# Kernel optimization log

Hardware: AMD Instinct MI355X
Metric: run time of the kernel (lower is better)

## Reference

```python
import jax, jax.numpy as jnp
import numpy as np

B, LC, LQ, D = 64, 512, 64, 256

def setup_inputs() -> dict:
    key = jax.random.key(0)
    k1, k2, k3, k4 = jax.random.split(key, 4)
    contex = jax.random.normal(k1, (B, LC, D), dtype=jnp.float32)
    question = jax.random.normal(k2, (B, LQ, D), dtype=jnp.float32)
    W_weight = jax.random.normal(k3, (1, 3 * D), dtype=jnp.float32) * (1.0 / np.sqrt(3 * D))
    W_bias = jax.random.normal(k4, (1,), dtype=jnp.float32) * 0.01
    return {"contex": contex, "question": question, "W_weight": W_weight, "W_bias": W_bias}

def reference(contex, question, W_weight, W_bias):
    d = contex.shape[-1]
    w = W_weight[0]  # [3D]; cat order in original is [q, c, q*c]
    wq, wc, wi = w[:d], w[d:2 * d], w[2 * d:]
    # S[b,i,j] = c_i.wc + q_j.wq + (c_i*q_j).wi + bias  (trilinear decomposition)
    s_c = contex @ wc                                   # [B, Lc]
    s_q = question @ wq                                 # [B, Lq]
    s_i = jnp.einsum('bid,bjd->bij', contex * wi, question)  # [B, Lc, Lq]
    S = s_i + s_c[:, :, None] + s_q[:, None, :] + W_bias[0]
    S1 = jax.nn.softmax(S, axis=2)                      # over question
    S2 = jax.nn.softmax(S, axis=1)                      # over context
    A = jnp.einsum('bij,bjd->bid', S1, question)        # [B, Lc, D]
    S3 = jnp.einsum('bij,bkj->bik', S1, S2)             # [B, Lc, Lc]
    Bm = jnp.einsum('bik,bkd->bid', S3, contex)         # [B, Lc, D]
    out = jnp.concatenate([contex, A, contex * A, contex * Bm], axis=2)  # [B, Lc, 4D]
    return out  # dropout is identity at inference
```

## Files before the change

kernel.cpp:

```cpp
#include <hip/hip_runtime.h>

#define BB 64
#define LCC 512
#define LQQ 64
#define DDD 256

typedef short bf16x8 __attribute__((ext_vector_type(8)));
typedef float f32x4 __attribute__((ext_vector_type(4)));

__device__ __forceinline__ unsigned short f2bf(float f) {
  union { float f; unsigned u; } v; v.f = f;
  unsigned u = v.u;
  return (unsigned short)((u + 0x7fffu + ((u >> 16) & 1u)) >> 16);
}
__device__ __forceinline__ float bf2f(unsigned u16) {
  union { unsigned u; float f; } v; v.u = u16 << 16;
  return v.f;
}

__global__ __launch_bounds__(256) void k1_scores(
    const float* __restrict__ cx, const float* __restrict__ qu,
    const float* __restrict__ W, const float* __restrict__ Wb,
    unsigned short* __restrict__ E, unsigned short* __restrict__ Et,
    float* __restrict__ rinv)
{
  __shared__ float w_lds[768];
  __shared__ unsigned short As[128 * 72];
  __shared__ unsigned short Bs[64 * 72];
  __shared__ float E_lds[128 * 65];
  __shared__ float sc_lds[128];
  __shared__ float sq_lds[64];

  const int tid = threadIdx.x;
  const int b  = blockIdx.x >> 2;
  const int i0 = (blockIdx.x & 3) * 128;
  const int w = tid >> 6, lane = tid & 63, quad = lane >> 4, ln = lane & 15;

  for (int idx = tid; idx < 768; idx += 256) w_lds[idx] = W[idx];

  f32x4 acc[2][4];
#pragma unroll
  for (int a = 0; a < 2; ++a)
#pragma unroll
    for (int c = 0; c < 4; ++c) acc[a][c] = (f32x4){0.f, 0.f, 0.f, 0.f};

  float scp = 0.f;
  float sqp = 0.f;
  const int ai = tid >> 1, ah = tid & 1;
  const int bj = tid >> 2, bc = tid & 3;

  for (int kk = 0; kk < 4; ++kk) {
    __syncthreads();
    {
      const float4* src = (const float4*)(cx + ((size_t)(b * LCC + i0 + ai)) * DDD + kk * 64 + ah * 32);
      const float* wi = w_lds + 512 + kk * 64 + ah * 32;
      const float* wc = w_lds + 256 + kk * 64 + ah * 32;
      unsigned short* dst = As + ai * 72 + ah * 32;
#pragma unroll
      for (int u = 0; u < 8; ++u) {
        float4 v = src[u];
        scp += v.x * wc[u*4+0] + v.y * wc[u*4+1] + v.z * wc[u*4+2] + v.w * wc[u*4+3];
        ushort4 o;
        o.x = f2bf(v.x * wi[u*4+0]);
        o.y = f2bf(v.y * wi[u*4+1]);
        o.z = f2bf(v.z * wi[u*4+2]);
        o.w = f2bf(v.w * wi[u*4+3]);
        *(ushort4*)(dst + u * 4) = o;
      }
    }
    {
      const float4* src = (const float4*)(qu + ((size_t)(b * LQQ + bj)) * DDD + kk * 64 + bc * 16);
      const float* wq = w_lds + kk * 64 + bc * 16;
      unsigned short* dst = Bs + bj * 72 + bc * 16;
#pragma unroll
      for (int u = 0; u < 4; ++u) {
        float4 v = src[u];
        sqp += v.x * wq[u*4+0] + v.y * wq[u*4+1] + v.z * wq[u*4+2] + v.w * wq[u*4+3];
        ushort4 o = { f2bf(v.x), f2bf(v.y), f2bf(v.z), f2bf(v.w) };
        *(ushort4*)(dst + u * 4) = o;
      }
    }
    __syncthreads();
#pragma unroll
    for (int ks = 0; ks < 2; ++ks) {
      bf16x8 af[2];
#pragma unroll
      for (int tm = 0; tm < 2; ++tm)
        af[tm] = *(const bf16x8*)(As + (w * 32 + tm * 16 + ln) * 72 + ks * 32 + quad * 8);
#pragma unroll
      for (int tn = 0; tn < 4; ++tn) {
        bf16x8 bf = *(const bf16x8*)(Bs + (tn * 16 + ln) * 72 + ks * 32 + quad * 8);
#pragma unroll
        for (int tm = 0; tm < 2; ++tm)
          acc[tm][tn] = __builtin_amdgcn_mfma_f32_16x16x32_bf16(af[tm], bf, acc[tm][tn], 0, 0, 0);
      }
    }
  }

  __syncthreads();
  w_lds[tid] = scp;
  w_lds[256 + tid] = sqp;
  __syncthreads();
  if (tid < 128) sc_lds[tid] = w_lds[2*tid] + w_lds[2*tid+1];
  if (tid < 64)
    sq_lds[tid] = w_lds[256 + 4*tid] + w_lds[256 + 4*tid+1]
                + w_lds[256 + 4*tid+2] + w_lds[256 + 4*tid+3];
  const float bias = Wb[0];
  __syncthreads();

#pragma unroll
  for (int tm = 0; tm < 2; ++tm)
#pragma unroll
    for (int tn = 0; tn < 4; ++tn)
#pragma unroll
      for (int r = 0; r < 4; ++r) {
        int il = w * 32 + tm * 16 + quad * 4 + r;
        int j  = tn * 16 + ln;
        float e = __expf(acc[tm][tn][r] + sc_lds[il] + sq_lds[j] + bias);
        E_lds[il * 65 + j] = e;
      }
  __syncthreads();
  {
    float s = 0.f;
#pragma unroll
    for (int j = 0; j < 32; ++j) s += E_lds[ai * 65 + ah * 32 + j];
    w_lds[tid] = s;
  }
  __syncthreads();
  if (tid < 128) rinv[b * LCC + i0 + tid] = 1.0f / (w_lds[2*tid] + w_lds[2*tid+1]);

  {
    unsigned short* dst = E + ((size_t)(b * LCC + i0 + ai)) * 64 + ah * 32;
    const float* srcr = E_lds + ai * 65 + ah * 32;
#pragma unroll
    for (int u = 0; u < 8; ++u) {
      ushort4 o = { f2bf(srcr[u*4+0]), f2bf(srcr[u*4+1]), f2bf(srcr[u*4+2]), f2bf(srcr[u*4+3]) };
      *(ushort4*)(dst + u * 4) = o;
    }
  }
  {
    unsigned short* dst = Et + ((size_t)(b * LQQ + bj)) * LCC + i0 + bc * 32;
#pragma unroll
    for (int u = 0; u < 8; ++u) {
      ushort4 o;
      o.x = f2bf(E_lds[(bc*32 + u*4 + 0) * 65 + bj]);
      o.y = f2bf(E_lds[(bc*32 + u*4 + 1) * 65 + bj]);
      o.z = f2bf(E_lds[(bc*32 + u*4 + 2) * 65 + bj]);
      o.w = f2bf(E_lds[(bc*32 + u*4 + 3) * 65 + bj]);
      *(ushort4*)(dst + u * 4) = o;
    }
  }
}

__global__ __launch_bounds__(256) void k2_tmat(
    const float* __restrict__ cx, const float* __restrict__ qu,
    const unsigned short* __restrict__ Et,
    unsigned short* __restrict__ Qt, unsigned short* __restrict__ Tt)
{
  __shared__ unsigned short As2[64 * 72];
  __shared__ unsigned short Bs2[64 * 72];
  __shared__ float Tl[64 * 65];
  __shared__ float cs_lds[64];

  const int tid = threadIdx.x;
  const int b  = blockIdx.x >> 2;
  const int d0 = (blockIdx.x & 3) * 64;
  const int w = tid >> 6, lane = tid & 63, quad = lane >> 4, ln = lane & 15;

  {
    const int j = tid >> 2, c = tid & 3;
    const float4* src = (const float4*)(qu + ((size_t)(b * LQQ + j)) * DDD + d0 + c * 16);
#pragma unroll
    for (int u = 0; u < 4; ++u) {
      float4 v = src[u];
      Tl[j * 65 + c*16 + u*4 + 0] = v.x;
      Tl[j * 65 + c*16 + u*4 + 1] = v.y;
      Tl[j * 65 + c*16 + u*4 + 2] = v.z;
      Tl[j * 65 + c*16 + u*4 + 3] = v.w;
    }
  }
  __syncthreads();
  {
    const int d = tid & 63, cj = tid >> 6;
    unsigned short* dst = Qt + ((size_t)(b * DDD + d0 + d)) * 64 + cj * 16;
#pragma unroll
    for (int u = 0; u < 4; ++u) {
      ushort4 o;
      o.x = f2bf(Tl[(cj*16 + u*4 + 0) * 65 + d]);
      o.y = f2bf(Tl[(cj*16 + u*4 + 1) * 65 + d]);
      o.z = f2bf(Tl[(cj*16 + u*4 + 2) * 65 + d]);
      o.w = f2bf(Tl[(cj*16 + u*4 + 3) * 65 + d]);
      *(ushort4*)(dst + u * 4) = o;
    }
  }

  f32x4 acc[4];
#pragma unroll
  for (int c = 0; c < 4; ++c) acc[c] = (f32x4){0.f, 0.f, 0.f, 0.f};
  float csp = 0.f;

  const int sj = tid >> 2, sc = tid & 3;
  const int si = tid & 63, sc2 = tid >> 6;

  for (int kk = 0; kk < 8; ++kk) {
    __syncthreads();
    {
      const uint4* src = (const uint4*)(Et + ((size_t)(b * LQQ + sj)) * LCC + kk * 64 + sc * 16);
#pragma unroll
      for (int u = 0; u < 2; ++u) {
        uint4 raw = src[u];
        *(uint4*)(As2 + sj * 72 + sc * 16 + u * 8) = raw;
        csp += bf2f(raw.x & 0xffffu) + bf2f(raw.x >> 16)
             + bf2f(raw.y & 0xffffu) + bf2f(raw.y >> 16)
             + bf2f(raw.z & 0xffffu) + bf2f(raw.z >> 16)
             + bf2f(raw.w & 0xffffu) + bf2f(raw.w >> 16);
      }
    }
    {
      const float4* src = (const float4*)(cx + ((size_t)(b * LCC + kk * 64 + si)) * DDD + d0 + sc2 * 16);
#pragma unroll
      for (int u = 0; u < 4; ++u) {
        float4 v = src[u];
        Bs2[(sc2*16 + u*4 + 0) * 72 + si] = f2bf(v.x);
        Bs2[(sc2*16 + u*4 + 1) * 72 + si] = f2bf(v.y);
        Bs2[(sc2*16 + u*4 + 2) * 72 + si] = f2bf(v.z);
        Bs2[(sc2*16 + u*4 + 3) * 72 + si] = f2bf(v.w);
      }
    }
    __syncthreads();
#pragma unroll
    for (int ks = 0; ks < 2; ++ks) {
      bf16x8 af = *(const bf16x8*)(As2 + (w * 16 + ln) * 72 + ks * 32 + quad * 8);
#pragma unroll
      for (int tn = 0; tn < 4; ++tn) {
        bf16x8 bf = *(const bf16x8*)(Bs2 + (tn * 16 + ln) * 72 + ks * 32 + quad * 8);
        acc[tn] = __builtin_amdgcn_mfma_f32_16x16x32_bf16(af, bf, acc[tn], 0, 0, 0);
      }
    }
  }

  __syncthreads();
  Tl[tid] = csp;
  __syncthreads();
  if (tid < 64) {
    float s = Tl[4*tid] + Tl[4*tid+1] + Tl[4*tid+2] + Tl[4*tid+3];
    cs_lds[tid] = 1.0f / s;
  }
  __syncthreads();
#pragma unroll
  for (int tn = 0; tn < 4; ++tn)
#pragma unroll
    for (int r = 0; r < 4; ++r) {
      int jl = w * 16 + quad * 4 + r;
      Tl[jl * 65 + tn * 16 + ln] = acc[tn][r] * cs_lds[jl];
    }
  __syncthreads();
  {
    const int d = tid & 63, cj = tid >> 6;
    unsigned short* dst = Tt + ((size_t)(b * DDD + d0 + d)) * 64 + cj * 16;
#pragma unroll
    for (int u = 0; u < 4; ++u) {
      ushort4 o;
      o.x = f2bf(Tl[(cj*16 + u*4 + 0) * 65 + d]);
      o.y = f2bf(Tl[(cj*16 + u*4 + 1) * 65 + d]);
      o.z = f2bf(Tl[(cj*16 + u*4 + 2) * 65 + d]);
      o.w = f2bf(Tl[(cj*16 + u*4 + 3) * 65 + d]);
      *(ushort4*)(dst + u * 4) = o;
    }
  }
}

__global__ __launch_bounds__(256) void k3_out(
    const float* __restrict__ cx,
    const unsigned short* __restrict__ E,
    const unsigned short* __restrict__ Qt,
    const unsigned short* __restrict__ Tt,
    const float* __restrict__ rinv,
    float* __restrict__ out)
{
  __shared__ unsigned short As3[64 * 72];
  __shared__ char BsTr[256 * 72 * 2];
  __shared__ float ri_lds[64];
  unsigned short* Bs3 = (unsigned short*)BsTr;
  float* Tr = (float*)BsTr;

  const int tid = threadIdx.x;
  const int bid = blockIdx.x;
  const int b    = bid >> 4;
  const int it   = (bid >> 1) & 7;
  const int half = bid & 1;
  const int i0 = it * 64;
  const int w = tid >> 6, lane = tid & 63, quad = lane >> 4, ln = lane & 15;

  {
    const int i = tid >> 2, c = tid & 3;
    const uint4* src = (const uint4*)(E + ((size_t)(b * LCC + i0 + i)) * 64 + c * 16);
#pragma unroll
    for (int u = 0; u < 2; ++u)
      *(uint4*)(As3 + i * 72 + c * 16 + u * 8) = src[u];
  }
  {
    const unsigned short* Bsrc = half ? Tt : Qt;
    const int nb = tid & 63, c2 = tid >> 6;
#pragma unroll
    for (int rr = 0; rr < 4; ++rr) {
      int n = rr * 64 + nb;
      const uint4* src = (const uint4*)(Bsrc + ((size_t)(b * DDD + n)) * 64 + c2 * 16);
#pragma unroll
      for (int u = 0; u < 2; ++u)
        *(uint4*)(Bs3 + n * 72 + c2 * 16 + u * 8) = src[u];
    }
  }
  if (tid < 64) ri_lds[tid] = rinv[b * LCC + i0 + tid];
  __syncthreads();

  f32x4 acc[4][4];
#pragma unroll
  for (int a = 0; a < 4; ++a)
#pragma unroll
    for (int c = 0; c < 4; ++c) acc[a][c] = (f32x4){0.f, 0.f, 0.f, 0.f};

#pragma unroll
  for (int ks = 0; ks < 2; ++ks) {
    bf16x8 af[4], bf[4];
#pragma unroll
    for (int tm = 0; tm < 4; ++tm)
      af[tm] = *(const bf16x8*)(As3 + (tm * 16 + ln) * 72 + ks * 32 + quad * 8);
#pragma unroll
    for (int tn = 0; tn < 4; ++tn)
      bf[tn] = *(const bf16x8*)(Bs3 + (w * 64 + tn * 16 + ln) * 72 + ks * 32 + quad * 8);
#pragma unroll
    for (int tm = 0; tm < 4; ++tm)
#pragma unroll
      for (int tn = 0; tn < 4; ++tn)
        acc[tm][tn] = __builtin_amdgcn_mfma_f32_16x16x32_bf16(af[tm], bf[tn], acc[tm][tn], 0, 0, 0);
  }

  const float* cxb = cx + (size_t)b * LCC * DDD;
  float* ob = out + (size_t)b * LCC * 1024;
  const int row = tid >> 4;
  const int fq  = tid & 15;

#pragma unroll
  for (int tm = 0; tm < 4; ++tm) {
    __syncthreads();
#pragma unroll
    for (int tn = 0; tn < 4; ++tn)
#pragma unroll
      for (int r = 0; r < 4; ++r) {
        int rloc = quad * 4 + r;
        Tr[rloc * 260 + w * 64 + tn * 16 + ln] = acc[tm][tn][r] * ri_lds[tm * 16 + rloc];
      }
    __syncthreads();
    const int i = i0 + tm * 16 + row;
#pragma unroll
    for (int u = 0; u < 4; ++u) {
      int c0 = (fq + u * 16) * 4;
      float4 v = *(const float4*)(Tr + row * 260 + c0);
      float4 c = *(const float4*)(cxb + (size_t)i * DDD + c0);
      float4 cv = { c.x * v.x, c.y * v.y, c.z * v.z, c.w * v.w };
      if (half == 0) {
        *(float4*)(ob + (size_t)i * 1024 + 256 + c0) = v;
        *(float4*)(ob + (size_t)i * 1024 + 512 + c0) = cv;
      } else {
        *(float4*)(ob + (size_t)i * 1024 + c0)       = c;
        *(float4*)(ob + (size_t)i * 1024 + 768 + c0) = cv;
      }
    }
  }
}

extern "C" void kernel_launch(void* const* d_in, const int* in_sizes, int n_in,
                              void* d_out, int out_size, void* d_ws, size_t ws_size,
                              hipStream_t stream) {
  const float* cx = (const float*)d_in[0];
  const float* qu = (const float*)d_in[1];
  const float* W  = (const float*)d_in[2];
  const float* Wb = (const float*)d_in[3];
  float* out = (float*)d_out;

  char* wsb = (char*)d_ws;
  unsigned short* E   = (unsigned short*)(wsb);
  unsigned short* Et  = (unsigned short*)(wsb + (4ull << 20));
  unsigned short* Qt  = (unsigned short*)(wsb + (8ull << 20));
  unsigned short* Tt  = (unsigned short*)(wsb + (10ull << 20));
  float*          ri  = (float*)(wsb + (12ull << 20));

  k1_scores<<<dim3(256), dim3(256), 0, stream>>>(cx, qu, W, Wb, E, Et, ri);
  k2_tmat  <<<dim3(256), dim3(256), 0, stream>>>(cx, qu, Et, Qt, Tt);
  k3_out   <<<dim3(1024), dim3(256), 0, stream>>>(cx, E, Qt, Tt, ri, out);
}
```

Baseline: 199.6 us.

## Double grid sizes of score and T kernels and load MFMA fragments directly from global

The score and T-matrix kernels now use 512 blocks with half-size tiles: 64 context rows per block in k1 and 32 feature columns per block in k2. k1 stages all of the question tile in LDS once, then each lane loads its context A fragment straight from global memory and converts it to bf16 in registers, so the per-k LDS staging loop and its barriers are gone. k2 and k3 also read their E/Et/Qt/Tt MFMA fragments directly from global instead of staging them in LDS. The intent is more parallelism and fewer barriers and LDS round trips. The cost is less coalesced, strided global fragment loads and some repeated loads across blocks.

Result: no change. 198.9 us (-0.4%).

```diff
diff --git a/kernel.cpp b/kernel.cpp
--- a/kernel.cpp
+++ b/kernel.cpp
@@ -8,13 +8,13 @@
 typedef short bf16x8 __attribute__((ext_vector_type(8)));
 typedef float f32x4 __attribute__((ext_vector_type(4)));
 
-__device__ __forceinline__ unsigned short f2bf(float f) {
+static __device__ __forceinline__ unsigned short f2bf(float f) {
   union { float f; unsigned u; } v; v.f = f;
   unsigned u = v.u;
   return (unsigned short)((u + 0x7fffu + ((u >> 16) & 1u)) >> 16);
 }
-__device__ __forceinline__ float bf2f(unsigned u16) {
-  union { unsigned u; float f; } v; v.u = u16 << 16;
+static __device__ __forceinline__ float bf2f(unsigned u16) {
+  union { unsigned u; float f; } v; v.u = (u16 & 0xffffu) << 16;
   return v.f;
 }
 
@@ -25,128 +25,118 @@
     float* __restrict__ rinv)
 {
   __shared__ float w_lds[768];
-  __shared__ unsigned short As[128 * 72];
-  __shared__ unsigned short Bs[64 * 72];
-  __shared__ float E_lds[128 * 65];
-  __shared__ float sc_lds[128];
+  __shared__ unsigned short Bs[64 * 264];
+  __shared__ float E_lds[64 * 65];
+  __shared__ float red[256];
+  __shared__ float sc_lds[64];
   __shared__ float sq_lds[64];
 
   const int tid = threadIdx.x;
-  const int b  = blockIdx.x >> 2;
-  const int i0 = (blockIdx.x & 3) * 128;
+  const int b  = blockIdx.x >> 3;
+  const int i0 = (blockIdx.x & 7) * 64;
   const int w = tid >> 6, lane = tid & 63, quad = lane >> 4, ln = lane & 15;
 
   for (int idx = tid; idx < 768; idx += 256) w_lds[idx] = W[idx];
-
-  f32x4 acc[2][4];
-#pragma unroll
-  for (int a = 0; a < 2; ++a)
-#pragma unroll
-    for (int c = 0; c < 4; ++c) acc[a][c] = (f32x4){0.f, 0.f, 0.f, 0.f};
+  __syncthreads();
+
+  {
+    const int bj = tid >> 2, bc = tid & 3;
+    const float4* src = (const float4*)(qu + ((size_t)(b * LQQ + bj)) * DDD + bc * 64);
+    const float* wq = w_lds + bc * 64;
+    unsigned short* dst = Bs + bj * 264 + bc * 64;
+    float sqp = 0.f;
+#pragma unroll
+    for (int u = 0; u < 16; ++u) {
+      float4 v = src[u];
+      sqp += v.x * wq[u*4+0] + v.y * wq[u*4+1] + v.z * wq[u*4+2] + v.w * wq[u*4+3];
+      ushort4 o = { f2bf(v.x), f2bf(v.y), f2bf(v.z), f2bf(v.w) };
+      *(ushort4*)(dst + u * 4) = o;
+    }
+    red[tid] = sqp;
+  }
+  __syncthreads();
+  if (tid < 64) sq_lds[tid] = red[4*tid] + red[4*tid+1] + red[4*tid+2] + red[4*tid+3];
+
+  f32x4 acc[4];
+#pragma unroll
+  for (int c = 0; c < 4; ++c) acc[c] = (f32x4){0.f, 0.f, 0.f, 0.f};
 
   float scp = 0.f;
-  float sqp = 0.f;
-  const int ai = tid >> 1, ah = tid & 1;
-  const int bj = tid >> 2, bc = tid & 3;
-
-  for (int kk = 0; kk < 4; ++kk) {
-    __syncthreads();
-    {
-      const float4* src = (const float4*)(cx + ((size_t)(b * LCC + i0 + ai)) * DDD + kk * 64 + ah * 32);
-      const float* wi = w_lds + 512 + kk * 64 + ah * 32;
-      const float* wc = w_lds + 256 + kk * 64 + ah * 32;
-      unsigned short* dst = As + ai * 72 + ah * 32;
-#pragma unroll
-      for (int u = 0; u < 8; ++u) {
-        float4 v = src[u];
-        scp += v.x * wc[u*4+0] + v.y * wc[u*4+1] + v.z * wc[u*4+2] + v.w * wc[u*4+3];
-        ushort4 o;
-        o.x = f2bf(v.x * wi[u*4+0]);
-        o.y = f2bf(v.y * wi[u*4+1]);
-        o.z = f2bf(v.z * wi[u*4+2]);
-        o.w = f2bf(v.w * wi[u*4+3]);
-        *(ushort4*)(dst + u * 4) = o;
+  const float* cxrow = cx + ((size_t)(b * LCC + i0 + w * 16 + ln)) * DDD;
+#pragma unroll
+  for (int kk = 0; kk < 4; ++kk)
+#pragma unroll
+    for (int ks = 0; ks < 2; ++ks) {
+      const int k0 = kk * 64 + ks * 32 + quad * 8;
+      float4 c0 = *(const float4*)(cxrow + k0);
+      float4 c1 = *(const float4*)(cxrow + k0 + 4);
+      const float* wcp = w_lds + 256 + k0;
+      const float* wip = w_lds + 512 + k0;
+      scp += c0.x*wcp[0] + c0.y*wcp[1] + c0.z*wcp[2] + c0.w*wcp[3]
+           + c1.x*wcp[4] + c1.y*wcp[5] + c1.z*wcp[6] + c1.w*wcp[7];
+      bf16x8 af;
+      af[0] = (short)f2bf(c0.x * wip[0]);
+      af[1] = (short)f2bf(c0.y * wip[1]);
+      af[2] = (short)f2bf(c0.z * wip[2]);
+      af[3] = (short)f2bf(c0.w * wip[3]);
+      af[4] = (short)f2bf(c1.x * wip[4]);
+      af[5] = (short)f2bf(c1.y * wip[5]);
+      af[6] = (short)f2bf(c1.z * wip[6]);
+      af[7] = (short)f2bf(c1.w * wip[7]);
+#pragma unroll
+      for (int tn = 0; tn < 4; ++tn) {
+        bf16x8 bf = *(const bf16x8*)(Bs + (tn * 16 + ln) * 264 + k0);
+        acc[tn] = __builtin_amdgcn_mfma_f32_16x16x32_bf16(af, bf, acc[tn], 0, 0, 0);
       }
     }
-    {
-      const float4* src = (const float4*)(qu + ((size_t)(b * LQQ + bj)) * DDD + kk * 64 + bc * 16);
-      const float* wq = w_lds + kk * 64 + bc * 16;
-      unsigned short* dst = Bs + bj * 72 + bc * 16;
-#pragma unroll
-      for (int u = 0; u < 4; ++u) {
-        float4 v = src[u];
-        sqp += v.x * wq[u*4+0] + v.y * wq[u*4+1] + v.z * wq[u*4+2] + v.w * wq[u*4+3];
-        ushort4 o = { f2bf(v.x), f2bf(v.y), f2bf(v.z), f2bf(v.w) };
-        *(ushort4*)(dst + u * 4) = o;
-      }
-    }
-    __syncthreads();
-#pragma unroll
-    for (int ks = 0; ks < 2; ++ks) {
-      bf16x8 af[2];
-#pragma unroll
-      for (int tm = 0; tm < 2; ++tm)
-        af[tm] = *(const bf16x8*)(As + (w * 32 + tm * 16 + ln) * 72 + ks * 32 + quad * 8);
-#pragma unroll
-      for (int tn = 0; tn < 4; ++tn) {
-        bf16x8 bf = *(const bf16x8*)(Bs + (tn * 16 + ln) * 72 + ks * 32 + quad * 8);
-#pragma unroll
-        for (int tm = 0; tm < 2; ++tm)
-          acc[tm][tn] = __builtin_amdgcn_mfma_f32_16x16x32_bf16(af[tm], bf, acc[tm][tn], 0, 0, 0);
-      }
-    }
-  }
-
-  __syncthreads();
-  w_lds[tid] = scp;
-  w_lds[256 + tid] = sqp;
-  __syncthreads();
-  if (tid < 128) sc_lds[tid] = w_lds[2*tid] + w_lds[2*tid+1];
+
+  __syncthreads();
+  red[(w * 16 + ln) * 4 + quad] = scp;
+  __syncthreads();
   if (tid < 64)
-    sq_lds[tid] = w_lds[256 + 4*tid] + w_lds[256 + 4*tid+1]
-                + w_lds[256 + 4*tid+2] + w_lds[256 + 4*tid+3];
-  const float bias = Wb[0];
-  __syncthreads();
-
-#pragma unroll
-  for (int tm = 0; tm < 2; ++tm)
-#pragma unroll
-    for (int tn = 0; tn < 4; ++tn)
-#pragma unroll
-      for (int r = 0; r < 4; ++r) {
-        int il = w * 32 + tm * 16 + quad * 4 + r;
-        int j  = tn * 16 + ln;
-        float e = __expf(acc[tm][tn][r] + sc_lds[il] + sq_lds[j] + bias);
-        E_lds[il * 65 + j] = e;
-      }
-  __syncthreads();
-  {
+    sc_lds[tid] = red[4*tid] + red[4*tid+1] + red[4*tid+2] + red[4*tid+3] + Wb[0];
+  __syncthreads();
+
+#pragma unroll
+  for (int tn = 0; tn < 4; ++tn)
+#pragma unroll
+    for (int r = 0; r < 4; ++r) {
+      int il = w * 16 + quad * 4 + r;
+      int j  = tn * 16 + ln;
+      E_lds[il * 65 + j] = __expf(acc[tn][r] + sc_lds[il] + sq_lds[j]);
+    }
+  __syncthreads();
+  {
+    const int i = tid >> 2, c = tid & 3;
     float s = 0.f;
 #pragma unroll
-    for (int j = 0; j < 32; ++j) s += E_lds[ai * 65 + ah * 32 + j];
-    w_lds[tid] = s;
-  }
-  __syncthreads();
-  if (tid < 128) rinv[b * LCC + i0 + tid] = 1.0f / (w_lds[2*tid] + w_lds[2*tid+1]);
-
-  {
-    unsigned short* dst = E + ((size_t)(b * LCC + i0 + ai)) * 64 + ah * 32;
-    const float* srcr = E_lds + ai * 65 + ah * 32;
-#pragma unroll
-    for (int u = 0; u < 8; ++u) {
+    for (int j = 0; j < 16; ++j) s += E_lds[i * 65 + c * 16 + j];
+    red[tid] = s;
+  }
+  __syncthreads();
+  if (tid < 64)
+    rinv[b * LCC + i0 + tid] = 1.0f / (red[4*tid] + red[4*tid+1] + red[4*tid+2] + red[4*tid+3]);
+
+  {
+    const int i = tid >> 2, c = tid & 3;
+    unsigned short* dst = E + ((size_t)(b * LCC + i0 + i)) * 64 + c * 16;
+    const float* srcr = E_lds + i * 65 + c * 16;
+#pragma unroll
+    for (int u = 0; u < 4; ++u) {
       ushort4 o = { f2bf(srcr[u*4+0]), f2bf(srcr[u*4+1]), f2bf(srcr[u*4+2]), f2bf(srcr[u*4+3]) };
       *(ushort4*)(dst + u * 4) = o;
     }
   }
   {
-    unsigned short* dst = Et + ((size_t)(b * LQQ + bj)) * LCC + i0 + bc * 32;
-#pragma unroll
-    for (int u = 0; u < 8; ++u) {
+    const int j = tid >> 2, c = tid & 3;
+    unsigned short* dst = Et + ((size_t)(b * LQQ + j)) * LCC + i0 + c * 16;
+#pragma unroll
+    for (int u = 0; u < 4; ++u) {
       ushort4 o;
-      o.x = f2bf(E_lds[(bc*32 + u*4 + 0) * 65 + bj]);
-      o.y = f2bf(E_lds[(bc*32 + u*4 + 1) * 65 + bj]);
-      o.z = f2bf(E_lds[(bc*32 + u*4 + 2) * 65 + bj]);
-      o.w = f2bf(E_lds[(bc*32 + u*4 + 3) * 65 + bj]);
+      o.x = f2bf(E_lds[(c*16 + u*4 + 0) * 65 + j]);
+      o.y = f2bf(E_lds[(c*16 + u*4 + 1) * 65 + j]);
+      o.z = f2bf(E_lds[(c*16 + u*4 + 2) * 65 + j]);
+      o.w = f2bf(E_lds[(c*16 + u*4 + 3) * 65 + j]);
       *(ushort4*)(dst + u * 4) = o;
     }
   }
@@ -157,116 +147,97 @@
     const unsigned short* __restrict__ Et,
     unsigned short* __restrict__ Qt, unsigned short* __restrict__ Tt)
 {
-  __shared__ unsigned short As2[64 * 72];
-  __shared__ unsigned short Bs2[64 * 72];
-  __shared__ float Tl[64 * 65];
-  __shared__ float cs_lds[64];
+  __shared__ unsigned short Bs2[32 * 72];
+  __shared__ float Tl[64 * 37];
+  __shared__ float red2[256];
+  __shared__ float csinv[64];
 
   const int tid = threadIdx.x;
-  const int b  = blockIdx.x >> 2;
-  const int d0 = (blockIdx.x & 3) * 64;
+  const int b  = blockIdx.x >> 3;
+  const int d0 = (blockIdx.x & 7) * 32;
   const int w = tid >> 6, lane = tid & 63, quad = lane >> 4, ln = lane & 15;
 
   {
     const int j = tid >> 2, c = tid & 3;
-    const float4* src = (const float4*)(qu + ((size_t)(b * LQQ + j)) * DDD + d0 + c * 16);
-#pragma unroll
-    for (int u = 0; u < 4; ++u) {
-      float4 v = src[u];
-      Tl[j * 65 + c*16 + u*4 + 0] = v.x;
-      Tl[j * 65 + c*16 + u*4 + 1] = v.y;
-      Tl[j * 65 + c*16 + u*4 + 2] = v.z;
-      Tl[j * 65 + c*16 + u*4 + 3] = v.w;
-    }
-  }
-  __syncthreads();
-  {
-    const int d = tid & 63, cj = tid >> 6;
-    unsigned short* dst = Qt + ((size_t)(b * DDD + d0 + d)) * 64 + cj * 16;
-#pragma unroll
-    for (int u = 0; u < 4; ++u) {
-      ushort4 o;
-      o.x = f2bf(Tl[(cj*16 + u*4 + 0) * 65 + d]);
-      o.y = f2bf(Tl[(cj*16 + u*4 + 1) * 65 + d]);
-      o.z = f2bf(Tl[(cj*16 + u*4 + 2) * 65 + d]);
-      o.w = f2bf(Tl[(cj*16 + u*4 + 3) * 65 + d]);
-      *(ushort4*)(dst + u * 4) = o;
-    }
-  }
-
-  f32x4 acc[4];
-#pragma unroll
-  for (int c = 0; c < 4; ++c) acc[c] = (f32x4){0.f, 0.f, 0.f, 0.f};
+    const float* srow = qu + ((size_t)(b * LQQ + j)) * DDD + d0 + c * 8;
+    float4 v0 = *(const float4*)srow;
+    float4 v1 = *(const float4*)(srow + 4);
+    float* t = Tl + j * 37 + c * 8;
+    t[0]=v0.x; t[1]=v0.y; t[2]=v0.z; t[3]=v0.w;
+    t[4]=v1.x; t[5]=v1.y; t[6]=v1.z; t[7]=v1.w;
+  }
+  __syncthreads();
+  {
+    const int d = tid >> 3, cj = tid & 7;
+    unsigned short* dst = Qt + ((size_t)(b * DDD + d0 + d)) * 64 + cj * 8;
+    ushort4 o0 = { f2bf(Tl[(cj*8+0)*37+d]), f2bf(Tl[(cj*8+1)*37+d]),
+                   f2bf(Tl[(cj*8+2)*37+d]), f2bf(Tl[(cj*8+3)*37+d]) };
+    ushort4 o1 = { f2bf(Tl[(cj*8+4)*37+d]), f2bf(Tl[(cj*8+5)*37+d]),
+                   f2bf(Tl[(cj*8+6)*37+d]), f2bf(Tl[(cj*8+7)*37+d]) };
+    *(ushort4*)dst = o0;
+    *(ushort4*)(dst + 4) = o1;
+  }
+
+  f32x4 acc[2];
+  acc[0] = (f32x4){0.f, 0.f, 0.f, 0.f};
+  acc[1] = (f32x4){0.f, 0.f, 0.f, 0.f};
   float csp = 0.f;
-
-  const int sj = tid >> 2, sc = tid & 3;
+  const unsigned short* etrow = Et + ((size_t)(b * LQQ + w * 16 + ln)) * LCC;
   const int si = tid & 63, sc2 = tid >> 6;
 
   for (int kk = 0; kk < 8; ++kk) {
     __syncthreads();
     {
-      const uint4* src = (const uint4*)(Et + ((size_t)(b * LQQ + sj)) * LCC + kk * 64 + sc * 16);
-#pragma unroll
-      for (int u = 0; u < 2; ++u) {
-        uint4 raw = src[u];
-        *(uint4*)(As2 + sj * 72 + sc * 16 + u * 8) = raw;
-        csp += bf2f(raw.x & 0xffffu) + bf2f(raw.x >> 16)
-             + bf2f(raw.y & 0xffffu) + bf2f(raw.y >> 16)
-             + bf2f(raw.z & 0xffffu) + bf2f(raw.z >> 16)
-             + bf2f(raw.w & 0xffffu) + bf2f(raw.w >> 16);
-      }
-    }
-    {
-      const float4* src = (const float4*)(cx + ((size_t)(b * LCC + kk * 64 + si)) * DDD + d0 + sc2 * 16);
-#pragma unroll
-      for (int u = 0; u < 4; ++u) {
-        float4 v = src[u];
-        Bs2[(sc2*16 + u*4 + 0) * 72 + si] = f2bf(v.x);
-        Bs2[(sc2*16 + u*4 + 1) * 72 + si] = f2bf(v.y);
-        Bs2[(sc2*16 + u*4 + 2) * 72 + si] = f2bf(v.z);
-        Bs2[(sc2*16 + u*4 + 3) * 72 + si] = f2bf(v.w);
-      }
-    }
+      const float* srow = cx + ((size_t)(b * LCC + kk * 64 + si)) * DDD + d0 + sc2 * 8;
+      float4 v0 = *(const float4*)srow;
+      float4 v1 = *(const float4*)(srow + 4);
+      Bs2[(sc2*8+0)*72 + si] = f2bf(v0.x);
+      Bs2[(sc2*8+1)*72 + si] = f2bf(v0.y);
+      Bs2[(sc2*8+2)*72 + si] = f2bf(v0.z);
+      Bs2[(sc2*8+3)*72 + si] = f2bf(v0.w);
+      Bs2[(sc2*8+4)*72 + si] = f2bf(v1.x);
+      Bs2[(sc2*8+5)*72 + si] = f2bf(v1.y);
+      Bs2[(sc2*8+6)*72 + si] = f2bf(v1.z);
+      Bs2[(sc2*8+7)*72 + si] = f2bf(v1.w);
+    }
+    bf16x8 af0 = *(const bf16x8*)(etrow + kk * 64 + quad * 8);
+    bf16x8 af1 = *(const bf16x8*)(etrow + kk * 64 + 32 + quad * 8);
+#pragma unroll
+    for (int e = 0; e < 8; ++e)
+      csp += bf2f((unsigned short)af0[e]) + bf2f((unsigned short)af1[e]);
     __syncthreads();
 #pragma unroll
-    for (int ks = 0; ks < 2; ++ks) {
-      bf16x8 af = *(const bf16x8*)(As2 + (w * 16 + ln) * 72 + ks * 32 + quad * 8);
-#pragma unroll
-      for (int tn = 0; tn < 4; ++tn) {
-        bf16x8 bf = *(const bf16x8*)(Bs2 + (tn * 16 + ln) * 72 + ks * 32 + quad * 8);
-        acc[tn] = __builtin_amdgcn_mfma_f32_16x16x32_bf16(af, bf, acc[tn], 0, 0, 0);
-      }
-    }
-  }
-
-  __syncthreads();
-  Tl[tid] = csp;
-  __syncthreads();
-  if (tid < 64) {
-    float s = Tl[4*tid] + Tl[4*tid+1] + Tl[4*tid+2] + Tl[4*tid+3];
-    cs_lds[tid] = 1.0f / s;
-  }
-  __syncthreads();
-#pragma unroll
-  for (int tn = 0; tn < 4; ++tn)
+    for (int tn = 0; tn < 2; ++tn) {
+      bf16x8 bf0 = *(const bf16x8*)(Bs2 + (tn * 16 + ln) * 72 + quad * 8);
+      bf16x8 bf1 = *(const bf16x8*)(Bs2 + (tn * 16 + ln) * 72 + 32 + quad * 8);
+      acc[tn] = __builtin_amdgcn_mfma_f32_16x16x32_bf16(af0, bf0, acc[tn], 0, 0, 0);
+      acc[tn] = __builtin_amdgcn_mfma_f32_16x16x32_bf16(af1, bf1, acc[tn], 0, 0, 0);
+    }
+  }
+
+  __syncthreads();
+  red2[(w * 16 + ln) * 4 + quad] = csp;
+  __syncthreads();
+  if (tid < 64)
+    csinv[tid] = 1.0f / (red2[4*tid] + red2[4*tid+1] + red2[4*tid+2] + red2[4*tid+3]);
+  __syncthreads();
+#pragma unroll
+  for (int tn = 0; tn < 2; ++tn)
 #pragma unroll
     for (int r = 0; r < 4; ++r) {
-      int jl = w * 16 + quad * 4 + r;
-      Tl[jl * 65 + tn * 16 + ln] = acc[tn][r] * cs_lds[jl];
-    }
-  __syncthreads();
-  {
-    const int d = tid & 63, cj = tid >> 6;
-    unsigned short* dst = Tt + ((size_t)(b * DDD + d0 + d)) * 64 + cj * 16;
-#pragma unroll
-    for (int u = 0; u < 4; ++u) {
-      ushort4 o;
-      o.x = f2bf(Tl[(cj*16 + u*4 + 0) * 65 + d]);
-      o.y = f2bf(Tl[(cj*16 + u*4 + 1) * 65 + d]);
-      o.z = f2bf(Tl[(cj*16 + u*4 + 2) * 65 + d]);
-      o.w = f2bf(Tl[(cj*16 + u*4 + 3) * 65 + d]);
-      *(ushort4*)(dst + u * 4) = o;
-    }
+      int j = w * 16 + quad * 4 + r;
+      Tl[j * 37 + tn * 16 + ln] = acc[tn][r] * csinv[j];
+    }
+  __syncthreads();
+  {
+    const int d = tid >> 3, cj = tid & 7;
+    unsigned short* dst = Tt + ((size_t)(b * DDD + d0 + d)) * 64 + cj * 8;
+    ushort4 o0 = { f2bf(Tl[(cj*8+0)*37+d]), f2bf(Tl[(cj*8+1)*37+d]),
+                   f2bf(Tl[(cj*8+2)*37+d]), f2bf(Tl[(cj*8+3)*37+d]) };
+    ushort4 o1 = { f2bf(Tl[(cj*8+4)*37+d]), f2bf(Tl[(cj*8+5)*37+d]),
+                   f2bf(Tl[(cj*8+6)*37+d]), f2bf(Tl[(cj*8+7)*37+d]) };
+    *(ushort4*)dst = o0;
+    *(ushort4*)(dst + 4) = o1;
   }
 }
 
@@ -278,11 +249,8 @@
     const float* __restrict__ rinv,
     float* __restrict__ out)
 {
-  __shared__ unsigned short As3[64 * 72];
-  __shared__ char BsTr[256 * 72 * 2];
+  __shared__ float Tr[16 * 260];
   __shared__ float ri_lds[64];
-  unsigned short* Bs3 = (unsigned short*)BsTr;
-  float* Tr = (float*)BsTr;
 
   const int tid = threadIdx.x;
   const int bid = blockIdx.x;
@@ -292,27 +260,10 @@
   const int i0 = it * 64;
   const int w = tid >> 6, lane = tid & 63, quad = lane >> 4, ln = lane & 15;
 
-  {
-    const int i = tid >> 2, c = tid & 3;
-    const uint4* src = (const uint4*)(E + ((size_t)(b * LCC + i0 + i)) * 64 + c * 16);
-#pragma unroll
-    for (int u = 0; u < 2; ++u)
-      *(uint4*)(As3 + i * 72 + c * 16 + u * 8) = src[u];
-  }
-  {
-    const unsigned short* Bsrc = half ? Tt : Qt;
-    const int nb = tid & 63, c2 = tid >> 6;
-#pragma unroll
-    for (int rr = 0; rr < 4; ++rr) {
-      int n = rr * 64 + nb;
-      const uint4* src = (const uint4*)(Bsrc + ((size_t)(b * DDD + n)) * 64 + c2 * 16);
-#pragma unroll
-      for (int u = 0; u < 2; ++u)
-        *(uint4*)(Bs3 + n * 72 + c2 * 16 + u * 8) = src[u];
-    }
-  }
   if (tid < 64) ri_lds[tid] = rinv[b * LCC + i0 + tid];
-  __syncthreads();
+
+  const unsigned short* Bsrc = (half ? Tt : Qt) + (size_t)b * DDD * 64;
+  const unsigned short* ebase = E + ((size_t)(b * LCC + i0)) * 64;
 
   f32x4 acc[4][4];
 #pragma unroll
@@ -322,18 +273,17 @@
 
 #pragma unroll
   for (int ks = 0; ks < 2; ++ks) {
-    bf16x8 af[4], bf[4];
+    bf16x8 af[4];
 #pragma unroll
     for (int tm = 0; tm < 4; ++tm)
-      af[tm] = *(const bf16x8*)(As3 + (tm * 16 + ln) * 72 + ks * 32 + quad * 8);
-#pragma unroll
-    for (int tn = 0; tn < 4; ++tn)
-      bf[tn] = *(const bf16x8*)(Bs3 + (w * 64 + tn * 16 + ln) * 72 + ks * 32 + quad * 8);
-#pragma unroll
-    for (int tm = 0; tm < 4; ++tm)
-#pragma unroll
-      for (int tn = 0; tn < 4; ++tn)
-        acc[tm][tn] = __builtin_amdgcn_mfma_f32_16x16x32_bf16(af[tm], bf[tn], acc[tm][tn], 0, 0, 0);
+      af[tm] = *(const bf16x8*)(ebase + (tm * 16 + ln) * 64 + ks * 32 + quad * 8);
+#pragma unroll
+    for (int tn = 0; tn < 4; ++tn) {
+      bf16x8 bf = *(const bf16x8*)(Bsrc + ((size_t)(w * 64 + tn * 16 + ln)) * 64 + ks * 32 + quad * 8);
+#pragma unroll
+      for (int tm = 0; tm < 4; ++tm)
+        acc[tm][tn] = __builtin_amdgcn_mfma_f32_16x16x32_bf16(af[tm], bf, acc[tm][tn], 0, 0, 0);
+    }
   }
 
   const float* cxb = cx + (size_t)b * LCC * DDD;
@@ -341,9 +291,9 @@
   const int row = tid >> 4;
   const int fq  = tid & 15;
 
+  __syncthreads();
 #pragma unroll
   for (int tm = 0; tm < 4; ++tm) {
-    __syncthreads();
 #pragma unroll
     for (int tn = 0; tn < 4; ++tn)
 #pragma unroll
@@ -367,6 +317,7 @@
         *(float4*)(ob + (size_t)i * 1024 + 768 + c0) = cv;
       }
     }
+    __syncthreads();
   }
 }
 
@@ -386,7 +337,7 @@
   unsigned short* Tt  = (unsigned short*)(wsb + (10ull << 20));
   float*          ri  = (float*)(wsb + (12ull << 20));
 
-  k1_scores<<<dim3(256), dim3(256), 0, stream>>>(cx, qu, W, Wb, E, Et, ri);
-  k2_tmat  <<<dim3(256), dim3(256), 0, stream>>>(cx, qu, Et, Qt, Tt);
+  k1_scores<<<dim3(512), dim3(256), 0, stream>>>(cx, qu, W, Wb, E, Et, ri);
+  k2_tmat  <<<dim3(512), dim3(256), 0, stream>>>(cx, qu, Et, Qt, Tt);
   k3_out   <<<dim3(1024), dim3(256), 0, stream>>>(cx, E, Qt, Tt, ri, out);
 }
```
